# Performance work log

Hardware: AMD Instinct MI355X
Metric: run time of the kernel (lower is better)

## Reference

```python
import jax, jax.numpy as jnp
import numpy as np

B, T, D, H = 8, 4096, 1024, 1024


def setup_inputs() -> dict:
    key = jax.random.key(0)
    ks = jax.random.split(key, 8)
    s = 1.0 / np.sqrt(D)
    x = jax.random.normal(ks[0], (B, T, D), dtype=jnp.float32)
    Wq = jax.random.uniform(ks[1], (H, D), jnp.float32, -s, s)
    bq = jax.random.uniform(ks[2], (H,), jnp.float32, -s, s)
    Wk = jax.random.uniform(ks[3], (H, D), jnp.float32, -s, s)
    bk = jax.random.uniform(ks[4], (H,), jnp.float32, -s, s)
    Wv = jax.random.uniform(ks[5], (H, D), jnp.float32, -s, s)
    bv = jax.random.uniform(ks[6], (H,), jnp.float32, -s, s)
    wbias = jax.random.uniform(ks[7], (H,), jnp.float32, 0.0, 1.0)  # torch.rand
    return {"x": x, "Wq": Wq, "bq": bq, "Wk": Wk, "bk": bk, "Wv": Wv, "bv": bv, "wbias": wbias}


def reference(x, Wq, bq, Wk, bk, Wv, bv, wbias):
    # Q, K, V: [B, T, H]
    Q = jnp.einsum('btd,hd->bth', x, Wq) + bq
    K = jnp.einsum('btd,hd->bth', x, Wk) + bk
    V = jnp.einsum('btd,hd->bth', x, Wv) + bv
    Q_sig = jax.nn.sigmoid(Q)
    numer = jnp.exp(K + wbias)            # [B, T, H]
    denom = numer.sum(axis=0)             # [T, H] (faithful: sum over batch axis)
    weighted = (numer * V).sum(axis=0) / denom  # [T, H]
    Yt = Q_sig * weighted                 # broadcast -> [B, T, H]
    return Yt  # to_out is Identity since dim == hidden_dim
```

## Files before the change

kernel.cpp:

```cpp
#include <hip/hip_runtime.h>
#include <hip/hip_bf16.h>

#define B_ 8
#define T_ 4096
#define D_ 1024
#define H_ 1024

typedef __attribute__((ext_vector_type(8))) short short8;
typedef __attribute__((ext_vector_type(4))) float floatx4;

#define GLOAD16(gptr, lptr) \
  __builtin_amdgcn_global_load_lds((const __attribute__((address_space(1))) void*)(gptr), \
                                   (__attribute__((address_space(3))) void*)(lptr), 16, 0, 0)

__device__ __forceinline__ ushort f2b(float f) {
  unsigned x = __builtin_bit_cast(unsigned, f);
  unsigned r = (x + 0x7fffu + ((x >> 16) & 1u)) >> 16;
  return (ushort)r;
}
__device__ __forceinline__ float b2f(ushort u) {
  return __builtin_bit_cast(float, (unsigned)u << 16);
}

__global__ void cvt_kernel(const float* __restrict__ in, ushort* __restrict__ out, int n) {
  int idx = blockIdx.x * blockDim.x + threadIdx.x;
  int stride = gridDim.x * blockDim.x;
  for (long i = (long)idx * 8; i < n; i += (long)stride * 8) {
    const float4 f0 = *(const float4*)(in + i);
    const float4 f1 = *(const float4*)(in + i + 4);
    union { ushort u[8]; uint4 v; } r;
    r.u[0] = f2b(f0.x); r.u[1] = f2b(f0.y); r.u[2] = f2b(f0.z); r.u[3] = f2b(f0.w);
    r.u[4] = f2b(f1.x); r.u[5] = f2b(f1.y); r.u[6] = f2b(f1.z); r.u[7] = f2b(f1.w);
    *(uint4*)(out + i) = r.v;
  }
}

__global__ void cvt3_kernel(const float* __restrict__ w0, const float* __restrict__ w1,
                            const float* __restrict__ w2, ushort* __restrict__ out, int n) {
  const float* in = (blockIdx.y == 0) ? w0 : (blockIdx.y == 1) ? w1 : w2;
  ushort* o = out + (size_t)blockIdx.y * n;
  int idx = blockIdx.x * blockDim.x + threadIdx.x;
  int stride = gridDim.x * blockDim.x;
  for (long i = (long)idx * 8; i < n; i += (long)stride * 8) {
    const float4 f0 = *(const float4*)(in + i);
    const float4 f1 = *(const float4*)(in + i + 4);
    union { ushort u[8]; uint4 v; } r;
    r.u[0] = f2b(f0.x); r.u[1] = f2b(f0.y); r.u[2] = f2b(f0.z); r.u[3] = f2b(f0.w);
    r.u[4] = f2b(f1.x); r.u[5] = f2b(f1.y); r.u[6] = f2b(f1.z); r.u[7] = f2b(f1.w);
    *(uint4*)(o + i) = r.v;
  }
}

template <int NCOLS, bool QEPI>
__global__ __launch_bounds__(512, 2) void gemm_bt(
    const ushort* __restrict__ Am, const ushort* __restrict__ Bm,
    ushort* __restrict__ KVout, const float* __restrict__ bq,
    const float* __restrict__ weighted, float* __restrict__ out) {
  extern __shared__ ushort lds[];

  const int tid = threadIdx.x;
  const int lane = tid & 63;
  const int w = tid >> 6;
  const int wr = w >> 2;
  const int wc = w & 3;
  const int R0 = blockIdx.x * 256;
  const int C0 = blockIdx.y * 256;

  const int r0 = tid >> 2;
  const int lc = (tid & 3) ^ ((tid >> 3) & 3);
  const ushort* asrc = Am + (size_t)(R0 + r0) * D_ + lc * 8;
  const ushort* bsrc = Bm + (size_t)(C0 + r0) * D_ + lc * 8;

  auto stage = [&](int t) {
    const int nb = t & 3;
    const int kt = t * 32;
    GLOAD16(asrc + kt, lds + nb * 8192 + tid * 8);
    GLOAD16(asrc + kt + (size_t)128 * D_, lds + nb * 8192 + (512 + tid) * 8);
    GLOAD16(bsrc + kt, lds + 32768 + nb * 8192 + tid * 8);
    GLOAD16(bsrc + kt + (size_t)128 * D_, lds + 32768 + nb * 8192 + (512 + tid) * 8);
  };

  const int baseA = wr * 128 + (lane & 15);
  const int baseB = wc * 64 + (lane & 15);
  const int aOff = baseA * 32 + ((lane >> 4) ^ ((baseA >> 1) & 3)) * 8;
  const int bOff = baseB * 32 + ((lane >> 4) ^ ((baseB >> 1) & 3)) * 8;

  floatx4 acc[8][4] = {};

  stage(0); stage(1);
  asm volatile("s_waitcnt vmcnt(4)" ::: "memory");
  __builtin_amdgcn_s_barrier();

  const int NT = D_ / 32;
  for (int t = 0; t < NT; ++t) {
    if (t < NT - 2) stage(t + 2);
    const ushort* Ab = lds + (t & 3) * 8192;
    const ushort* Bb = lds + 32768 + (t & 3) * 8192;

    short8 b[4], a[8];
#pragma unroll
    for (int n = 0; n < 4; ++n) b[n] = *(const short8*)(Bb + bOff + n * 512);
#pragma unroll
    for (int m = 0; m < 8; ++m) a[m] = *(const short8*)(Ab + aOff + m * 512);
#pragma unroll
    for (int m = 0; m < 8; ++m)
#pragma unroll
      for (int n = 0; n < 4; ++n)
        acc[m][n] = __builtin_amdgcn_mfma_f32_16x16x32_bf16(a[m], b[n], acc[m][n], 0, 0, 0);

    if (t < NT - 2) { asm volatile("s_waitcnt vmcnt(4)" ::: "memory"); }
    else            { asm volatile("s_waitcnt vmcnt(0)" ::: "memory"); }
    __builtin_amdgcn_s_barrier();
  }

  const int lrb = wr * 64 + (lane >> 4) * 4;
  const int lcol = wc * 64 + (lane & 15);
#pragma unroll
  for (int mh = 0; mh < 2; ++mh) {
    if (mh) __builtin_amdgcn_s_barrier();
    if constexpr (QEPI) {
      float* lf = (float*)lds;
#pragma unroll
      for (int mi = 0; mi < 4; ++mi)
#pragma unroll
        for (int n = 0; n < 4; ++n)
#pragma unroll
          for (int r = 0; r < 4; ++r)
            lf[(lrb + mi * 16 + r) * 256 + lcol + n * 16] = acc[mh * 4 + mi][n][r];
      __builtin_amdgcn_s_barrier();
#pragma unroll
      for (int j = 0; j < 16; ++j) {
        int cidx = j * 512 + tid;
        int lr = cidx >> 6;
        int cc = cidx & 63;
        int grow = R0 + (lr >> 6) * 128 + mh * 64 + (lr & 63);
        float4 v = *(float4*)(lf + lr * 256 + cc * 4);
        float4 bq4 = *(const float4*)(bq + C0 + cc * 4);
        float4 wv = *(const float4*)(weighted + (size_t)(grow & (T_ - 1)) * H_ + C0 + cc * 4);
        float4 o;
        o.x = wv.x / (1.f + __expf(-(v.x + bq4.x)));
        o.y = wv.y / (1.f + __expf(-(v.y + bq4.y)));
        o.z = wv.z / (1.f + __expf(-(v.z + bq4.z)));
        o.w = wv.w / (1.f + __expf(-(v.w + bq4.w)));
        *(float4*)(out + (size_t)grow * NCOLS + C0 + cc * 4) = o;
      }
    } else {
      ushort* lh = lds;
#pragma unroll
      for (int mi = 0; mi < 4; ++mi)
#pragma unroll
        for (int n = 0; n < 4; ++n)
#pragma unroll
          for (int r = 0; r < 4; ++r)
            lh[(lrb + mi * 16 + r) * 256 + lcol + n * 16] = f2b(acc[mh * 4 + mi][n][r]);
      __builtin_amdgcn_s_barrier();
#pragma unroll
      for (int j = 0; j < 8; ++j) {
        int cidx = j * 512 + tid;
        int lr = cidx >> 5;
        int cc = cidx & 31;
        int grow = R0 + (lr >> 6) * 128 + mh * 64 + (lr & 63);
        uint4 v = *(uint4*)(lh + lr * 256 + cc * 8);
        *(uint4*)(KVout + (size_t)grow * NCOLS + C0 + cc * 8) = v;
      }
    }
  }
}

__global__ __launch_bounds__(256) void reduce_kernel(
    const ushort* __restrict__ KV, const float* __restrict__ bk,
    const float* __restrict__ bv, const float* __restrict__ wb,
    float* __restrict__ weighted) {
  const int gid = blockIdx.x * 256 + threadIdx.x;
  const int t = gid >> 7;
  const int h0 = (gid & 127) * 8;

  float bk8[8], bv8[8], wb8[8];
#pragma unroll
  for (int j = 0; j < 8; ++j) {
    bk8[j] = bk[h0 + j];
    bv8[j] = bv[h0 + j];
    wb8[j] = wb[h0 + j];
  }

  float sn[8] = {}, sw[8] = {};
  for (int b = 0; b < B_; ++b) {
    const size_t rowoff = (size_t)(b * T_ + t) * (2 * H_);
    const short8 k8 = *(const short8*)(KV + rowoff + h0);
    const short8 v8 = *(const short8*)(KV + rowoff + H_ + h0);
#pragma unroll
    for (int j = 0; j < 8; ++j) {
      float e = __expf(b2f((ushort)k8[j]) + bk8[j] + wb8[j]);
      sn[j] += e;
      sw[j] += e * (b2f((ushort)v8[j]) + bv8[j]);
    }
  }
  float4 o0, o1;
  o0.x = sw[0] / sn[0]; o0.y = sw[1] / sn[1]; o0.z = sw[2] / sn[2]; o0.w = sw[3] / sn[3];
  o1.x = sw[4] / sn[4]; o1.y = sw[5] / sn[5]; o1.z = sw[6] / sn[6]; o1.w = sw[7] / sn[7];
  *(float4*)(weighted + (size_t)t * H_ + h0) = o0;
  *(float4*)(weighted + (size_t)t * H_ + h0 + 4) = o1;
}

extern "C" void kernel_launch(void* const* d_in, const int* in_sizes, int n_in,
                              void* d_out, int out_size, void* d_ws, size_t ws_size,
                              hipStream_t stream) {
  (void)in_sizes; (void)n_in; (void)out_size; (void)ws_size;
  const float* x = (const float*)d_in[0];
  const float* Wq = (const float*)d_in[1];
  const float* bq = (const float*)d_in[2];
  const float* Wk = (const float*)d_in[3];
  const float* bk = (const float*)d_in[4];
  const float* Wv = (const float*)d_in[5];
  const float* bv = (const float*)d_in[6];
  const float* wbias = (const float*)d_in[7];
  float* out = (float*)d_out;

  char* ws = (char*)d_ws;
  const size_t XN = (size_t)B_ * T_ * D_;
  const size_t WN = (size_t)H_ * D_;
  ushort* xb   = (ushort*)ws;
  ushort* Wqb  = (ushort*)(ws + XN * 2);
  ushort* Wkvb = Wqb + WN;
  float* weighted = (float*)(ws + XN * 2 + 3 * WN * 2);
  ushort* KV = (ushort*)(ws + XN * 2 + 3 * WN * 2 + (size_t)T_ * H_ * 4);

  (void)hipFuncSetAttribute((const void*)gemm_bt<2048, false>,
                            hipFuncAttributeMaxDynamicSharedMemorySize, 131072);
  (void)hipFuncSetAttribute((const void*)gemm_bt<1024, true>,
                            hipFuncAttributeMaxDynamicSharedMemorySize, 131072);

  cvt_kernel<<<2048, 256, 0, stream>>>(x, xb, (int)XN);
  cvt3_kernel<<<dim3(512, 3), 256, 0, stream>>>(Wq, Wk, Wv, Wqb, (int)WN);

  gemm_bt<2048, false><<<dim3((B_ * T_) / 256, 2048 / 256), 512, 131072, stream>>>(
      xb, Wkvb, KV, nullptr, nullptr, nullptr);
  reduce_kernel<<<(T_ * H_ / 8) / 256, 256, 0, stream>>>(KV, bk, bv, wbias, weighted);
  gemm_bt<1024, true><<<dim3((B_ * T_) / 256, 1024 / 256), 512, 131072, stream>>>(
      xb, Wqb, nullptr, bq, weighted, out);
}
```

Baseline: 329.5 us.

## Deepen GEMM pipeline with register double-buffered LDS fragments and MFMA priority

```diff
diff --git a/kernel.cpp b/kernel.cpp
--- a/kernel.cpp
+++ b/kernel.cpp
@@ -86,30 +86,55 @@
   const int bOff = baseB * 32 + ((lane >> 4) ^ ((baseB >> 1) & 3)) * 8;
 
   floatx4 acc[8][4] = {};
-
-  stage(0); stage(1);
+  short8 aP[4], aN[4], aS[4], bP[4], bN[4];
+
+  auto ldB = [&](short8* d, int tt) {
+    const ushort* Bb = lds + 32768 + (tt & 3) * 8192;
+#pragma unroll
+    for (int n = 0; n < 4; ++n) d[n] = *(const short8*)(Bb + bOff + n * 512);
+  };
+  auto ldA = [&](short8* d, int tt, int mo) {
+    const ushort* Ab = lds + (tt & 3) * 8192;
+#pragma unroll
+    for (int m = 0; m < 4; ++m) d[m] = *(const short8*)(Ab + aOff + (mo + m) * 512);
+  };
+  auto mm = [&](const short8* a4, const short8* b4, int mo) {
+#pragma unroll
+    for (int m = 0; m < 4; ++m)
+#pragma unroll
+      for (int n = 0; n < 4; ++n)
+        acc[mo + m][n] =
+            __builtin_amdgcn_mfma_f32_16x16x32_bf16(a4[m], b4[n], acc[mo + m][n], 0, 0, 0);
+  };
+
+  stage(0); stage(1); stage(2);
   asm volatile("s_waitcnt vmcnt(4)" ::: "memory");
   __builtin_amdgcn_s_barrier();
+  ldB(bP, 0); ldA(aP, 0, 0);
 
   const int NT = D_ / 32;
-  for (int t = 0; t < NT; ++t) {
-    if (t < NT - 2) stage(t + 2);
-    const ushort* Ab = lds + (t & 3) * 8192;
-    const ushort* Bb = lds + 32768 + (t & 3) * 8192;
-
-    short8 b[4], a[8];
-#pragma unroll
-    for (int n = 0; n < 4; ++n) b[n] = *(const short8*)(Bb + bOff + n * 512);
-#pragma unroll
-    for (int m = 0; m < 8; ++m) a[m] = *(const short8*)(Ab + aOff + m * 512);
-#pragma unroll
-    for (int m = 0; m < 8; ++m)
-#pragma unroll
-      for (int n = 0; n < 4; ++n)
-        acc[m][n] = __builtin_amdgcn_mfma_f32_16x16x32_bf16(a[m], b[n], acc[m][n], 0, 0, 0);
-
-    if (t < NT - 2) { asm volatile("s_waitcnt vmcnt(4)" ::: "memory"); }
+  for (int t = 0; t < NT; t += 2) {
+    if (t + 3 < NT) stage(t + 3);
+    ldA(aS, t, 4);
+    ldB(bN, t + 1);
+    ldA(aN, t + 1, 0);
+    __builtin_amdgcn_s_setprio(1);
+    mm(aP, bP, 0);
+    mm(aS, bP, 4);
+    __builtin_amdgcn_s_setprio(0);
+    if (t < NT - 3) { asm volatile("s_waitcnt vmcnt(4)" ::: "memory"); }
     else            { asm volatile("s_waitcnt vmcnt(0)" ::: "memory"); }
+    __builtin_amdgcn_s_barrier();
+
+    if (t + 4 < NT) stage(t + 4);
+    ldA(aS, t + 1, 4);
+    if (t + 2 < NT) { ldB(bP, t + 2); ldA(aP, t + 2, 0); }
+    __builtin_amdgcn_s_setprio(1);
+    mm(aN, bN, 0);
+    mm(aS, bN, 4);
+    __builtin_amdgcn_s_setprio(0);
+    if (t + 1 < NT - 3) { asm volatile("s_waitcnt vmcnt(4)" ::: "memory"); }
+    else                { asm volatile("s_waitcnt vmcnt(0)" ::: "memory"); }
     __builtin_amdgcn_s_barrier();
   }
 
```

New measurement: 324.8 us. No clear change (-1.4%).
